# Kernel tuning notes

Hardware: AMD Instinct MI355X
Metric: run time of the kernel (lower is better)

The kernel has to match this reference:

```python
import jax, jax.numpy as jnp
import numpy as np

IN_SIZE = 1024
HID = 1024


def setup_inputs() -> dict:
    key = jax.random.key(0)
    ks = jax.random.split(key, 8)
    B = 8192
    comb = IN_SIZE + 2 * HID
    scale = 1.0 / np.sqrt(comb)
    inp = {
        "x": jax.random.normal(ks[0], (B, IN_SIZE), jnp.float32),
        "h_left": jax.random.normal(ks[1], (B, HID), jnp.float32),
        "c_left": jax.random.normal(ks[2], (B, HID), jnp.float32),
        "h_right": jax.random.normal(ks[3], (B, HID), jnp.float32),
        "c_right": jax.random.normal(ks[4], (B, HID), jnp.float32),
        # Stacked weights for the 5 gates: [i, f_left, f_right, o, u]
        "W": jax.random.uniform(ks[5], (5 * HID, comb), jnp.float32, -scale, scale),
        "b": jax.random.uniform(ks[6], (5 * HID,), jnp.float32, -scale, scale),
    }
    return inp


def reference(x, h_left, c_left, h_right, c_right, W, b):
    # combined: (B, input_size + 2*hidden_size)
    combined = jnp.concatenate([x, h_left, h_right], axis=1)
    # One fused GEMM for all 5 gates: (B, 5H)
    gates = combined @ W.T + b
    i, fl, fr, o, u = jnp.split(gates, 5, axis=1)
    i = jax.nn.sigmoid(i)
    fl = jax.nn.sigmoid(fl)
    fr = jax.nn.sigmoid(fr)
    o = jax.nn.sigmoid(o)
    u = jnp.tanh(u)
    c = i * u + fl * c_left + fr * c_right
    h = o * jnp.tanh(c)
    return (h, c)
```

## Files before the change

kernel.cpp:

```cpp
#include <hip/hip_runtime.h>
#include <stdint.h>

typedef unsigned int u32;
typedef short short8 __attribute__((ext_vector_type(8)));
typedef short bf16x8 __attribute__((ext_vector_type(8)));
typedef float f32x4  __attribute__((ext_vector_type(4)));

#define B_ROWS 8192
#define HID    1024
#define KDIM   3072
#define NGATE  5

#define BM 256
#define BN 320
#define BK 64
#define NT (KDIM / BK)
#define LDSA_SH (BM * BK)
#define LDSB_SH (BN * BK)
#define BUF_SH  (LDSA_SH + LDSB_SH)
#define BUF_BYTES (BUF_SH * 2)

__device__ __forceinline__ short f2bf(float f) {
  u32 u = __builtin_bit_cast(u32, f);
  u += 0x7FFFu + ((u >> 16) & 1u);
  return (short)(u >> 16);
}

__device__ __forceinline__ float sigf(float v) { return 1.0f / (1.0f + __expf(-v)); }

__device__ __forceinline__ void async_copy16(const void* g, void* l) {
  __builtin_amdgcn_global_load_lds(
      (__attribute__((address_space(1))) void*)(g),
      (__attribute__((address_space(3))) void*)(l),
      16, 0, 0);
}

__global__ void convert_combined(const float* __restrict__ x,
                                 const float* __restrict__ hl,
                                 const float* __restrict__ hr,
                                 short* __restrict__ out) {
  const int total  = B_ROWS * (KDIM / 8);
  const int stride = gridDim.x * blockDim.x;
  for (int i = blockIdx.x * blockDim.x + threadIdx.x; i < total; i += stride) {
    int row = i / (KDIM / 8);
    int col = (i - row * (KDIM / 8)) * 8;
    const float* src;
    if (col < 1024)      src = x  + (int64_t)row * 1024 + col;
    else if (col < 2048) src = hl + (int64_t)row * 1024 + (col - 1024);
    else                 src = hr + (int64_t)row * 1024 + (col - 2048);
    float4 v0 = ((const float4*)src)[0];
    float4 v1 = ((const float4*)src)[1];
    short8 r;
    r[0] = f2bf(v0.x); r[1] = f2bf(v0.y); r[2] = f2bf(v0.z); r[3] = f2bf(v0.w);
    r[4] = f2bf(v1.x); r[5] = f2bf(v1.y); r[6] = f2bf(v1.z); r[7] = f2bf(v1.w);
    *(short8*)(out + (int64_t)row * KDIM + col) = r;
  }
}

__global__ void convert_w(const float* __restrict__ Wf, short* __restrict__ out) {
  const int total  = NGATE * HID * (KDIM / 8);
  const int stride = gridDim.x * blockDim.x;
  for (int i = blockIdx.x * blockDim.x + threadIdx.x; i < total; i += stride) {
    int64_t e = (int64_t)i * 8;
    float4 v0 = ((const float4*)(Wf + e))[0];
    float4 v1 = ((const float4*)(Wf + e))[1];
    short8 r;
    r[0] = f2bf(v0.x); r[1] = f2bf(v0.y); r[2] = f2bf(v0.z); r[3] = f2bf(v0.w);
    r[4] = f2bf(v1.x); r[5] = f2bf(v1.y); r[6] = f2bf(v1.z); r[7] = f2bf(v1.w);
    *(short8*)(out + e) = r;
  }
}

__global__ __launch_bounds__(512, 2) void lstm_gemm(
    const short* __restrict__ Abf,
    const short* __restrict__ Wbf,
    const float* __restrict__ bias,
    const float* __restrict__ c_left,
    const float* __restrict__ c_right,
    float* __restrict__ out) {
  __shared__ short lds[2 * BUF_SH];
  char* const ldsc = (char*)lds;

  const int tid = threadIdx.x;
  const int w  = tid >> 6;
  const int l  = tid & 63;
  const int wm = w >> 2;
  const int wn = w & 3;
  const int lc = l & 15;
  const int khalf = l >> 4;

  const int bid = blockIdx.x;
  const int wg  = (bid & 7) * 64 + (bid >> 3);
  const int m0  = (wg >> 4) * BM;
  const int j0  = (wg & 15) * 64;

  const int r8 = l >> 3;
  const int sl = (l & 7) ^ r8;
  u32 aoff[4], boff[5];
#pragma unroll
  for (int i = 0; i < 4; ++i)
    aoff[i] = (u32)(m0 + (w * 4 + i) * 8 + r8) * KDIM + sl * 8;
#pragma unroll
  for (int i = 0; i < 5; ++i) {
    int rb = (w * 5 + i) * 8 + r8;
    int g  = (rb % 80) >> 4;
    int dj = (rb / 80) * 16 + (rb & 15);
    boff[i] = (u32)(g * HID + j0 + dj) * KDIM + sl * 8;
  }

  const u32 sw0 = (u32)(((khalf    ) ^ (lc & 7)) * 16);
  const u32 sw1 = (u32)(((khalf + 4) ^ (lc & 7)) * 16);
  u32 aAd0 = (u32)((wm * 128 + lc) * 128) + sw0;
  u32 aAd1 = (u32)((wm * 128 + lc) * 128) + sw1;
  u32 bAd0 = (u32)(LDSA_SH * 2) + (u32)((wn * 80 + lc) * 128) + sw0;
  u32 bAd1 = (u32)(LDSA_SH * 2) + (u32)((wn * 80 + lc) * 128) + sw1;

  f32x4 acc[8][5];
  const f32x4 zero = {0.0f, 0.0f, 0.0f, 0.0f};
#pragma unroll
  for (int m = 0; m < 8; ++m)
#pragma unroll
    for (int n = 0; n < 5; ++n) acc[m][n] = zero;

#pragma unroll
  for (int i = 0; i < 4; ++i)
    async_copy16(Abf + aoff[i], lds + (w * 4 + i) * 512);
#pragma unroll
  for (int i = 0; i < 5; ++i)
    async_copy16(Wbf + boff[i], lds + LDSA_SH + (w * 5 + i) * 512);
#pragma unroll
  for (int i = 0; i < 4; ++i) aoff[i] += BK;
#pragma unroll
  for (int i = 0; i < 5; ++i) boff[i] += BK;
  asm volatile("s_waitcnt vmcnt(0)" ::: "memory");
  __syncthreads();

  int bufd = BUF_BYTES;
  for (int t = 0; t < NT; ++t) {
    bf16x8 bfr[5][2];
#pragma unroll
    for (int p = 0; p < 4; ++p) {
      if (p == 0) {
        if (t < NT - 1) {
          short* dA = lds + ((t + 1) & 1) * BUF_SH;
#pragma unroll
          for (int i = 0; i < 4; ++i)
            async_copy16(Abf + aoff[i], dA + (w * 4 + i) * 512);
        }
#pragma unroll
        for (int nf = 0; nf < 5; ++nf) {
          bfr[nf][0] = *(const bf16x8*)(ldsc + bAd0 + nf * 2048);
          bfr[nf][1] = *(const bf16x8*)(ldsc + bAd1 + nf * 2048);
        }
      }
      if (p == 2 && t < NT - 1) {
        short* dB = lds + ((t + 1) & 1) * BUF_SH + LDSA_SH;
#pragma unroll
        for (int i = 0; i < 5; ++i)
          async_copy16(Wbf + boff[i], dB + (w * 5 + i) * 512);
      }
      bf16x8 af[2][2];
#pragma unroll
      for (int mf = 0; mf < 2; ++mf) {
        af[mf][0] = *(const bf16x8*)(ldsc + aAd0 + (p * 32 + mf * 16) * 128);
        af[mf][1] = *(const bf16x8*)(ldsc + aAd1 + (p * 32 + mf * 16) * 128);
      }
      __builtin_amdgcn_s_barrier();
      __builtin_amdgcn_s_setprio(1);
#pragma unroll
      for (int mf = 0; mf < 2; ++mf)
#pragma unroll
        for (int nf = 0; nf < 5; ++nf)
#pragma unroll
          for (int kk = 0; kk < 2; ++kk)
            acc[p * 2 + mf][nf] = __builtin_amdgcn_mfma_f32_16x16x32_bf16(
                af[mf][kk], bfr[nf][kk], acc[p * 2 + mf][nf], 0, 0, 0);
      __builtin_amdgcn_s_setprio(0);
      if (p == 3)
        asm volatile("s_waitcnt vmcnt(0)" ::: "memory");
      __builtin_amdgcn_s_barrier();
    }
    aAd0 += bufd; aAd1 += bufd; bAd0 += bufd; bAd1 += bufd;
    bufd = -bufd;
#pragma unroll
    for (int i = 0; i < 4; ++i) aoff[i] += BK;
#pragma unroll
    for (int i = 0; i < 5; ++i) boff[i] += BK;
  }

  const int j = j0 + wn * 16 + lc;
  float bi[5];
#pragma unroll
  for (int g = 0; g < 5; ++g) bi[g] = bias[g * HID + j];
#pragma unroll
  for (int m = 0; m < 8; ++m) {
#pragma unroll
    for (int r = 0; r < 4; ++r) {
      const int row = m0 + wm * 128 + m * 16 + khalf * 4 + r;
      const int off = row * HID + j;
      float iv  = sigf(acc[m][0][r] + bi[0]);
      float flv = sigf(acc[m][1][r] + bi[1]);
      float frv = sigf(acc[m][2][r] + bi[2]);
      float ov  = sigf(acc[m][3][r] + bi[3]);
      float uv  = tanhf(acc[m][4][r] + bi[4]);
      float cv  = iv * uv + flv * c_left[off] + frv * c_right[off];
      out[off] = ov * tanhf(cv);
      out[B_ROWS * HID + off] = cv;
    }
  }
}

__global__ void lstm_fallback(const float* __restrict__ x, const float* __restrict__ hl,
                              const float* __restrict__ hr, const float* __restrict__ cl,
                              const float* __restrict__ cr, const float* __restrict__ W,
                              const float* __restrict__ b, float* __restrict__ out) {
  int64_t idx = (int64_t)blockIdx.x * blockDim.x + threadIdx.x;
  if (idx >= (int64_t)B_ROWS * HID) return;
  int bi = (int)(idx >> 10);
  int j  = (int)(idx & 1023);
  float acc[5];
#pragma unroll
  for (int g = 0; g < 5; ++g) acc[g] = b[g * HID + j];
  const float* segs[3] = {x + (int64_t)bi * 1024, hl + (int64_t)bi * 1024,
                          hr + (int64_t)bi * 1024};
  for (int s = 0; s < 3; ++s) {
    const float4* v = (const float4*)segs[s];
    for (int k4 = 0; k4 < 256; ++k4) {
      float4 a = v[k4];
#pragma unroll
      for (int g = 0; g < 5; ++g) {
        const float4 wv = *(const float4*)(W + (int64_t)(g * HID + j) * KDIM + s * 1024 + k4 * 4);
        acc[g] += a.x * wv.x + a.y * wv.y + a.z * wv.z + a.w * wv.w;
      }
    }
  }
  float iv = sigf(acc[0]), fl = sigf(acc[1]), fr = sigf(acc[2]), ov = sigf(acc[3]);
  float uv = tanhf(acc[4]);
  float cv = iv * uv + fl * cl[idx] + fr * cr[idx];
  out[idx] = ov * tanhf(cv);
  out[(int64_t)B_ROWS * HID + idx] = cv;
}

extern "C" void kernel_launch(void* const* d_in, const int* in_sizes, int n_in,
                              void* d_out, int out_size, void* d_ws, size_t ws_size,
                              hipStream_t stream) {
  const float* x  = (const float*)d_in[0];
  const float* hl = (const float*)d_in[1];
  const float* cl = (const float*)d_in[2];
  const float* hr = (const float*)d_in[3];
  const float* cr = (const float*)d_in[4];
  const float* W  = (const float*)d_in[5];
  const float* b  = (const float*)d_in[6];
  float* out = (float*)d_out;

  const size_t needA = (size_t)B_ROWS * KDIM * sizeof(short);
  const size_t needW = (size_t)NGATE * HID * KDIM * sizeof(short);

  if (ws_size >= needA + needW) {
    short* Abf = (short*)d_ws;
    short* Wbf = (short*)((char*)d_ws + needA);
    convert_combined<<<2048, 256, 0, stream>>>(x, hl, hr, Abf);
    convert_w<<<2048, 256, 0, stream>>>(W, Wbf);
    lstm_gemm<<<512, 512, 0, stream>>>(Abf, Wbf, b, cl, cr, out);
  } else {
    lstm_fallback<<<(B_ROWS * HID) / 256, 256, 0, stream>>>(x, hl, hr, cl, cr, W, b, out);
  }
}
```

Before: 298.7 us.

## Prefetch two K-tiles ahead into the buffer being consumed, staggering A loads

Deepens the global-to-LDS prefetch from one tile ahead to two, reusing the double buffer. After each phase barrier, loads for tile t+2 are written into the buffer of tile t, whose fragments have already been read into registers. A-tile loads are spread across phases by wave index so each wave overwrites only the rows consumed in that phase. The wait is relaxed to vmcnt(9) so one tile's loads stay in flight, which hides more memory latency. The cost is tighter correctness reasoning about buffer reuse and more outstanding loads.

```diff
diff --git a/kernel.cpp b/kernel.cpp
--- a/kernel.cpp
+++ b/kernel.cpp
@@ -86,6 +86,7 @@
   const int l  = tid & 63;
   const int wm = w >> 2;
   const int wn = w & 3;
+  const int wphase = w & 3;
   const int lc = l & 15;
   const int khalf = l >> 4;
 
@@ -132,33 +133,35 @@
   for (int i = 0; i < 4; ++i) aoff[i] += BK;
 #pragma unroll
   for (int i = 0; i < 5; ++i) boff[i] += BK;
-  asm volatile("s_waitcnt vmcnt(0)" ::: "memory");
-  __syncthreads();
+#pragma unroll
+  for (int i = 0; i < 4; ++i)
+    async_copy16(Abf + aoff[i], lds + BUF_SH + (w * 4 + i) * 512);
+#pragma unroll
+  for (int i = 0; i < 5; ++i)
+    async_copy16(Wbf + boff[i], lds + BUF_SH + LDSA_SH + (w * 5 + i) * 512);
+#pragma unroll
+  for (int i = 0; i < 4; ++i) aoff[i] += BK;
+#pragma unroll
+  for (int i = 0; i < 5; ++i) boff[i] += BK;
+  asm volatile("s_waitcnt vmcnt(9)" ::: "memory");
+  __builtin_amdgcn_s_barrier();
 
   int bufd = BUF_BYTES;
   for (int t = 0; t < NT; ++t) {
+    short* const dstA = lds + (t & 1) * BUF_SH;
+    short* const dstB = dstA + LDSA_SH;
+    const bool pre = (t < NT - 2);
     bf16x8 bfr[5][2];
+
 #pragma unroll
     for (int p = 0; p < 4; ++p) {
       if (p == 0) {
-        if (t < NT - 1) {
-          short* dA = lds + ((t + 1) & 1) * BUF_SH;
-#pragma unroll
-          for (int i = 0; i < 4; ++i)
-            async_copy16(Abf + aoff[i], dA + (w * 4 + i) * 512);
-        }
 #pragma unroll
         for (int nf = 0; nf < 5; ++nf) {
           bfr[nf][0] = *(const bf16x8*)(ldsc + bAd0 + nf * 2048);
           bfr[nf][1] = *(const bf16x8*)(ldsc + bAd1 + nf * 2048);
         }
       }
-      if (p == 2 && t < NT - 1) {
-        short* dB = lds + ((t + 1) & 1) * BUF_SH + LDSA_SH;
-#pragma unroll
-        for (int i = 0; i < 5; ++i)
-          async_copy16(Wbf + boff[i], dB + (w * 5 + i) * 512);
-      }
       bf16x8 af[2][2];
 #pragma unroll
       for (int mf = 0; mf < 2; ++mf) {
@@ -166,6 +169,19 @@
         af[mf][1] = *(const bf16x8*)(ldsc + aAd1 + (p * 32 + mf * 16) * 128);
       }
       __builtin_amdgcn_s_barrier();
+      __builtin_amdgcn_sched_barrier(0);
+      if (pre) {
+        if (p == 0) {
+#pragma unroll
+          for (int i = 0; i < 5; ++i)
+            async_copy16(Wbf + boff[i], dstB + (w * 5 + i) * 512);
+        }
+        if (wphase == p) {
+#pragma unroll
+          for (int i = 0; i < 4; ++i)
+            async_copy16(Abf + aoff[i], dstA + (w * 4 + i) * 512);
+        }
+      }
       __builtin_amdgcn_s_setprio(1);
 #pragma unroll
       for (int mf = 0; mf < 2; ++mf)
@@ -176,16 +192,20 @@
             acc[p * 2 + mf][nf] = __builtin_amdgcn_mfma_f32_16x16x32_bf16(
                 af[mf][kk], bfr[nf][kk], acc[p * 2 + mf][nf], 0, 0, 0);
       __builtin_amdgcn_s_setprio(0);
-      if (p == 3)
-        asm volatile("s_waitcnt vmcnt(0)" ::: "memory");
+      if (p == 3) {
+        if (t < NT - 2)       asm volatile("s_waitcnt vmcnt(9)" ::: "memory");
+        else if (t == NT - 2) asm volatile("s_waitcnt vmcnt(0)" ::: "memory");
+      }
       __builtin_amdgcn_s_barrier();
     }
     aAd0 += bufd; aAd1 += bufd; bAd0 += bufd; bAd1 += bufd;
     bufd = -bufd;
-#pragma unroll
-    for (int i = 0; i < 4; ++i) aoff[i] += BK;
-#pragma unroll
-    for (int i = 0; i < 5; ++i) boff[i] += BK;
+    if (pre) {
+#pragma unroll
+      for (int i = 0; i < 4; ++i) aoff[i] += BK;
+#pragma unroll
+      for (int i = 0; i < 5; ++i) boff[i] += BK;
+    }
   }
 
   const int j = j0 + wn * 16 + lc;
```

Result: slower. 316.0 us (+5.8%).
